# Kernel optimization log

Measured on AMD Instinct MI355X. Metric: run time of the kernel, lower is better.

The kernel has to match this reference:

```python
import jax, jax.numpy as jnp
import numpy as np

NUM_HEADS = 8
KERNEL = 7  # kernel_size (kh == kw == 7), dilation 1, non-causal


def _na_indices(L, k):
    # NATTEN neighborhood: window start clamped so the kxk window stays in-bounds
    starts = jnp.clip(jnp.arange(L) - k // 2, 0, L - k)  # [L]
    return starts[:, None] + jnp.arange(k)               # [L, k]


def setup_inputs() -> dict:
    key = jax.random.key(0)
    k1, k2, k3 = jax.random.split(key, 3)
    B, H, W, C = 1, 64, 128, 256
    x = jax.random.normal(k1, (B, H, W, C), dtype=jnp.float32)
    # weights stored as [in, out] so y = x @ w + b (equivalent to torch Linear math)
    w_qkv = jax.random.normal(k2, (C, 3 * C), dtype=jnp.float32) * 0.02
    b_qkv = jnp.zeros((3 * C,), dtype=jnp.float32)
    w_proj = jax.random.normal(k3, (C, C), dtype=jnp.float32) * 0.02
    b_proj = jnp.zeros((C,), dtype=jnp.float32)
    return {"x": x, "w_qkv": w_qkv, "b_qkv": b_qkv, "w_proj": w_proj, "b_proj": b_proj}


def reference(x, w_qkv, b_qkv, w_proj, b_proj):
    B, H, W, C = x.shape
    nh = NUM_HEADS
    hd = C // nh
    scale = hd ** -0.5
    kk = KERNEL

    qkv = (x @ w_qkv + b_qkv).reshape(B, H, W, 3, nh, hd)
    q = qkv[:, :, :, 0]  # [B,H,W,nh,hd]
    k = qkv[:, :, :, 1]
    v = qkv[:, :, :, 2]

    ih = _na_indices(H, kk)  # [H,kk]
    iw = _na_indices(W, kk)  # [W,kk]

    # gather K/V neighborhoods: [B,H,kh,W,kw,nh,hd]
    k_win = k[:, ih][:, :, :, iw]
    v_win = v[:, ih][:, :, :, iw]

    # scores: query vs its kh*kw neighbors
    attn = jnp.einsum('bhwnd,bhpwqnd->bhwnpq', q * scale, k_win)  # [B,H,W,nh,kh,kw]
    attn = jax.nn.softmax(attn.reshape(B, H, W, nh, kk * kk), axis=-1)
    attn = attn.reshape(B, H, W, nh, kk, kk)

    out = jnp.einsum('bhwnpq,bhpwqnd->bhwnd', attn, v_win)  # [B,H,W,nh,hd]
    out = out.reshape(B, H, W, C)
    return out @ w_proj + b_proj
```

## Files before the change

### kernel.cpp

```cpp
#include <hip/hip_runtime.h>
#include <cmath>

#define HH 64
#define WW 128
#define CC 256
#define NHEAD 8
#define HDIM 32
#define NPIX (HH*WW)
#define QKV_N (3*CC)

typedef __attribute__((ext_vector_type(8))) short short8v;
typedef __attribute__((ext_vector_type(4))) short short4v;
typedef __attribute__((ext_vector_type(4))) float f32x4;
typedef unsigned int u32;

__device__ __forceinline__ short f2bf(float f) {
    unsigned int u = __builtin_bit_cast(unsigned int, f);
    u += 0x7fffu + ((u >> 16) & 1u);
    return (short)(u >> 16);
}

__global__ __launch_bounds__(256)
void prep(const float* __restrict__ x, const float* __restrict__ w_qkv,
          const float* __restrict__ w_proj, short* __restrict__ x_bf,
          short* __restrict__ wqkv_t, short* __restrict__ wproj_t)
{
    __shared__ float tile[32][33];
    const int b = blockIdx.x;
    if (b < 1024) {
        const int i = b * 256 + threadIdx.x;
        float4 a = ((const float4*)x)[i * 2];
        float4 c = ((const float4*)x)[i * 2 + 1];
        short8v o;
        o[0] = f2bf(a.x); o[1] = f2bf(a.y); o[2] = f2bf(a.z); o[3] = f2bf(a.w);
        o[4] = f2bf(c.x); o[5] = f2bf(c.y); o[6] = f2bf(c.z); o[7] = f2bf(c.w);
        ((short8v*)x_bf)[i] = o;
        return;
    }
    const float* src; short* dst; int N, idx;
    if (b < 1216) { idx = b - 1024; src = w_qkv;  dst = wqkv_t;  N = QKV_N; }
    else          { idx = b - 1216; src = w_proj; dst = wproj_t; N = CC;    }
    const int nbx = N / 32;
    const int bn = (idx % nbx) * 32;
    const int bk = (idx / nbx) * 32;
    const int tx = threadIdx.x & 31, ty = threadIdx.x >> 5;
#pragma unroll
    for (int i = 0; i < 32; i += 8)
        tile[ty + i][tx] = src[(size_t)(bk + ty + i) * N + bn + tx];
    __syncthreads();
#pragma unroll
    for (int i = 0; i < 32; i += 8)
        dst[(size_t)(bn + ty + i) * CC + bk + tx] = f2bf(tile[tx][ty + i]);
}

template<int BM, int BN, bool OUT32>
__global__ __launch_bounds__(256)
void gemm_bf(const short* __restrict__ A, const short* __restrict__ Bt,
             const float* __restrict__ bias, void* __restrict__ Cv,
             int M, int N, int K)
{
    constexpr int BK  = 32;
    constexpr int NGA = BM * BK / 2048;
    constexpr int NGB = BN * BK / 2048;
    __shared__ short As[2][BM * BK];
    __shared__ short Bs[2][BN * BK];

    const int tid  = threadIdx.x;
    const int lane = tid & 63;
    const int wave = tid >> 6;
    constexpr int WM = BM / 2, WN = BN / 2;
    constexpr int FM = WM / 16, FN = WN / 16;
    const int wm0 = (wave >> 1) * WM;
    const int wn0 = (wave & 1) * WN;
    const int bm = blockIdx.x * BM, bn = blockIdx.y * BN;
    const int l15 = lane & 15, l4 = lane >> 4;

    f32x4 acc[FM][FN];
#pragma unroll
    for (int i = 0; i < FM; ++i)
#pragma unroll
        for (int j = 0; j < FN; ++j) acc[i][j] = (f32x4){0.f, 0.f, 0.f, 0.f};

    auto stage = [&](int buf, int t) {
#pragma unroll
        for (int i = 0; i < NGA; ++i) {
            const int g = tid + 256 * i;
            __builtin_amdgcn_global_load_lds(
                (const __attribute__((address_space(1))) u32*)
                    (A + (size_t)(bm + (g >> 2)) * K + t * BK + (g & 3) * 8),
                (__attribute__((address_space(3))) u32*)&As[buf][g * 8],
                16, 0, 0);
        }
#pragma unroll
        for (int i = 0; i < NGB; ++i) {
            const int g = tid + 256 * i;
            __builtin_amdgcn_global_load_lds(
                (const __attribute__((address_space(1))) u32*)
                    (Bt + (size_t)(bn + (g >> 2)) * K + t * BK + (g & 3) * 8),
                (__attribute__((address_space(3))) u32*)&Bs[buf][g * 8],
                16, 0, 0);
        }
    };

    stage(0, 0);
    const int NT = K / BK;

    for (int t = 0; t < NT; ++t) {
        const int cur = t & 1;
        __syncthreads();
        if (t + 1 < NT) stage(cur ^ 1, t + 1);

        short8v af[FM], bf[FN];
#pragma unroll
        for (int fm = 0; fm < FM; ++fm)
            af[fm] = *(const short8v*)&As[cur][(wm0 + fm * 16 + l15) * BK + l4 * 8];
#pragma unroll
        for (int fn = 0; fn < FN; ++fn)
            bf[fn] = *(const short8v*)&Bs[cur][(wn0 + fn * 16 + l15) * BK + l4 * 8];
#pragma unroll
        for (int fm = 0; fm < FM; ++fm)
#pragma unroll
            for (int fn = 0; fn < FN; ++fn)
                acc[fm][fn] = __builtin_amdgcn_mfma_f32_16x16x32_bf16(
                    af[fm], bf[fn], acc[fm][fn], 0, 0, 0);
    }

    const int col0 = bn + wn0 + l15;
    const int row0 = bm + wm0 + l4 * 4;
#pragma unroll
    for (int fn = 0; fn < FN; ++fn) {
        const float bv = bias[col0 + fn * 16];
#pragma unroll
        for (int fm = 0; fm < FM; ++fm)
#pragma unroll
            for (int r = 0; r < 4; ++r) {
                const size_t off = (size_t)(row0 + fm * 16 + r) * N + col0 + fn * 16;
                if (OUT32) ((float*)Cv)[off] = acc[fm][fn][r] + bv;
                else       ((short*)Cv)[off] = f2bf(acc[fm][fn][r] + bv);
            }
    }
}

#define KSLOT 248
#define LDK   40
#define VSLOT 264

__global__ __launch_bounds__(256)
void na_mfma(const short* __restrict__ qkv, short* __restrict__ attn)
{
    __shared__ short Ksh[KSLOT * LDK];
    __shared__ short Vsh[32 * VSLOT];

    const int x0 = blockIdx.x * 16;
    const int y0 = blockIdx.y * 4;
    const int head = blockIdx.z;
    const int tid = threadIdx.x, lane = tid & 63, w = tid >> 6;
    const int rs  = min(max(y0 - 3, 0), HH - 7);
    const int wsx = x0 - 3;

    for (int idx = tid; idx < 880; idx += 256) {
        int g = idx & 3, rc = idx >> 2;
        int i = rc / 22, c = rc - i * 22;
        int yy = rs + i, xx = wsx + c;
        if (yy < HH && (unsigned)xx < WW) {
            *(short8v*)&Ksh[(i * 24 + c) * LDK + g * 8] =
                *(const short8v*)(qkv + (size_t)(yy * WW + xx) * QKV_N
                                  + CC + head * HDIM + g * 8);
        }
    }
    for (int idx = tid; idx < 264; idx += 256) {
        int g = idx & 3, q2 = idx >> 2;
        int i = q2 / 6, cq = q2 - i * 6;
        int yy = rs + i;
        short8v vv[4];
#pragma unroll
        for (int j = 0; j < 4; ++j) {
            int c = cq * 4 + j, xx = wsx + c;
            if (yy < HH && c < 22 && (unsigned)xx < WW)
                vv[j] = *(const short8v*)(qkv + (size_t)(yy * WW + xx) * QKV_N
                                          + 2 * CC + head * HDIM + g * 8);
            else {
                short8v z = {0,0,0,0,0,0,0,0};
                vv[j] = z;
            }
        }
#pragma unroll
        for (int jd = 0; jd < 8; ++jd) {
            short4v s4 = {vv[0][jd], vv[1][jd], vv[2][jd], vv[3][jd]};
            *(short4v*)&Vsh[(g * 8 + jd) * VSLOT + i * 24 + cq * 4] = s4;
        }
    }

    const int l15 = lane & 15, l4 = lane >> 4;
    const int y = y0 + w;
    short8v qf = *(const short8v*)(qkv + (size_t)(y * WW + x0 + l15) * QKV_N
                                   + head * HDIM + l4 * 8);
    __syncthreads();

    const int wbase = (min(max(y - 3, 0), HH - 7) - rs) * 24;

    f32x4 sacc[11];
#pragma unroll
    for (int kc = 0; kc < 11; ++kc) {
        short8v kf = *(const short8v*)&Ksh[(wbase + kc * 16 + l15) * LDK + l4 * 8];
        f32x4 z = {0.f, 0.f, 0.f, 0.f};
        sacc[kc] = __builtin_amdgcn_mfma_f32_16x16x32_bf16(kf, qf, z, 0, 0, 0);
    }

    const int xq = x0 + l15;
    const int cw = min(max(xq - 3, 0), WW - 7) - wsx;
    const float scale = 0.17677669529663687f;
    float lsum = 0.f;
#pragma unroll
    for (int kc = 0; kc < 11; ++kc) {
#pragma unroll
        for (int r = 0; r < 4; ++r) {
            int kl = kc * 16 + l4 * 4 + r;
            int row = kl / 24;
            int c = kl - row * 24;
            bool valid = (row < 7) && (c >= cw) && (c <= cw + 6);
            float e = valid ? __expf(sacc[kc][r] * scale) : 0.f;
            sacc[kc][r] = e;
            lsum += e;
        }
    }
    lsum += __shfl_xor(lsum, 16);
    lsum += __shfl_xor(lsum, 32);
    const float inv = 1.0f / lsum;

    short4v pf[12];
#pragma unroll
    for (int kc = 0; kc < 11; ++kc) {
        short4v pk;
#pragma unroll
        for (int r = 0; r < 4; ++r) pk[r] = f2bf(sacc[kc][r] * inv);
        pf[kc] = pk;
    }
    pf[11] = (short4v){0, 0, 0, 0};

    const int src0 = ((l4 & 1) << 5) + l15;
    const int src1 = src0 + 16;
    const bool hi = (l4 & 2) != 0;
    f32x4 oacc[2];
    oacc[0] = (f32x4){0.f, 0.f, 0.f, 0.f};
    oacc[1] = (f32x4){0.f, 0.f, 0.f, 0.f};
#pragma unroll
    for (int kc2 = 0; kc2 < 6; ++kc2) {
        int lo0 = ((const int*)&pf[2 * kc2])[0];
        int lo1 = ((const int*)&pf[2 * kc2])[1];
        int hi0 = ((const int*)&pf[2 * kc2 + 1])[0];
        int hi1 = ((const int*)&pf[2 * kc2 + 1])[1];
        int a0 = __shfl(lo0, src0), a1 = __shfl(lo1, src0);
        int a2 = __shfl(lo0, src1), a3 = __shfl(lo1, src1);
        int b0 = __shfl(hi0, src0), b1 = __shfl(hi1, src0);
        int b2 = __shfl(hi0, src1), b3 = __shfl(hi1, src1);
        int w0 = hi ? b0 : a0, w1 = hi ? b1 : a1;
        int w2 = hi ? b2 : a2, w3 = hi ? b3 : a3;
        int wv[4] = {w0, w1, w2, w3};
        short8v bfrag = *(const short8v*)wv;
#pragma unroll
        for (int nc = 0; nc < 2; ++nc) {
            short8v vf = *(const short8v*)&Vsh[(nc * 16 + l15) * VSLOT
                                               + wbase + kc2 * 32 + l4 * 8];
            oacc[nc] = __builtin_amdgcn_mfma_f32_16x16x32_bf16(vf, bfrag, oacc[nc], 0, 0, 0);
        }
    }

    short* op = attn + (size_t)(y * WW + x0 + l15) * CC + head * HDIM;
#pragma unroll
    for (int nc = 0; nc < 2; ++nc) {
        short4v o;
#pragma unroll
        for (int r = 0; r < 4; ++r) o[r] = f2bf(oacc[nc][r]);
        *(short4v*)(op + nc * 16 + l4 * 4) = o;
    }
}

extern "C" void kernel_launch(void* const* d_in, const int* in_sizes, int n_in,
                              void* d_out, int out_size, void* d_ws, size_t ws_size,
                              hipStream_t stream)
{
    const float* x      = (const float*)d_in[0];
    const float* w_qkv  = (const float*)d_in[1];
    const float* b_qkv  = (const float*)d_in[2];
    const float* w_proj = (const float*)d_in[3];
    const float* b_proj = (const float*)d_in[4];
    float* out = (float*)d_out;

    char* ws = (char*)d_ws;
    short* qkv_bf  = (short*)ws;
    short* attn_bf = (short*)(ws + 12582912);
    short* x_bf    = (short*)(ws + 16777216);
    short* wqkv_t  = (short*)(ws + 20971520);
    short* wproj_t = (short*)(ws + 21364736);

    prep<<<dim3(1280), dim3(256), 0, stream>>>(x, w_qkv, w_proj,
                                               x_bf, wqkv_t, wproj_t);

    gemm_bf<128, 128, false><<<dim3(NPIX / 128, QKV_N / 128), dim3(256), 0, stream>>>(
        x_bf, wqkv_t, b_qkv, qkv_bf, NPIX, QKV_N, CC);

    na_mfma<<<dim3(WW / 16, HH / 4, NHEAD), dim3(256), 0, stream>>>(qkv_bf, attn_bf);

    gemm_bf<64, 128, true><<<dim3(NPIX / 64, CC / 128), dim3(256), 0, stream>>>(
        attn_bf, wproj_t, b_proj, out, NPIX, CC, CC);
}
```

Before: 41.62 us.

## Fuse x bf16 conversion into QKV GEMM, use head-major QKV layout, swizzle LDS

The fp32-to-bf16 conversion of x moves out of the prep kernel and into the QKV GEMM, which loads fp32 A tiles, converts them in registers and stores them to LDS. This removes a full write and reread of x in bf16. The QKV output is written head-major ([3*nh][NPIX][32]) so the neighborhood attention kernel reads contiguous 64-byte rows per pixel. Both GEMMs add an XOR swizzle on the LDS layout to cut bank conflicts. The QKV GEMM now uses 64x128 tiles with a single-buffered A tile and an extra barrier, and its scattered 2-byte stores into the head-major layout may hurt write efficiency.

```diff
diff --git a/kernel.cpp b/kernel.cpp
--- a/kernel.cpp
+++ b/kernel.cpp
@@ -9,6 +9,10 @@
 #define NPIX (HH*WW)
 #define QKV_N (3*CC)
 
+#define KSLOT 248
+#define LDK   40
+#define VSLOT 264
+
 typedef __attribute__((ext_vector_type(8))) short short8v;
 typedef __attribute__((ext_vector_type(4))) short short4v;
 typedef __attribute__((ext_vector_type(4))) float f32x4;
@@ -21,25 +25,14 @@
 }
 
 __global__ __launch_bounds__(256)
-void prep(const float* __restrict__ x, const float* __restrict__ w_qkv,
-          const float* __restrict__ w_proj, short* __restrict__ x_bf,
-          short* __restrict__ wqkv_t, short* __restrict__ wproj_t)
+void prep_w(const float* __restrict__ w_qkv, const float* __restrict__ w_proj,
+            short* __restrict__ wq_t, short* __restrict__ wp_t)
 {
     __shared__ float tile[32][33];
-    const int b = blockIdx.x;
-    if (b < 1024) {
-        const int i = b * 256 + threadIdx.x;
-        float4 a = ((const float4*)x)[i * 2];
-        float4 c = ((const float4*)x)[i * 2 + 1];
-        short8v o;
-        o[0] = f2bf(a.x); o[1] = f2bf(a.y); o[2] = f2bf(a.z); o[3] = f2bf(a.w);
-        o[4] = f2bf(c.x); o[5] = f2bf(c.y); o[6] = f2bf(c.z); o[7] = f2bf(c.w);
-        ((short8v*)x_bf)[i] = o;
-        return;
-    }
-    const float* src; short* dst; int N, idx;
-    if (b < 1216) { idx = b - 1024; src = w_qkv;  dst = wqkv_t;  N = QKV_N; }
-    else          { idx = b - 1216; src = w_proj; dst = wproj_t; N = CC;    }
+    int idx = blockIdx.x;
+    const float* src; short* dst; int N;
+    if (idx < 192) { src = w_qkv;  dst = wq_t; N = QKV_N; }
+    else { idx -= 192; src = w_proj; dst = wp_t; N = CC; }
     const int nbx = N / 32;
     const int bn = (idx % nbx) * 32;
     const int bk = (idx / nbx) * 32;
@@ -53,74 +46,153 @@
         dst[(size_t)(bn + ty + i) * CC + bk + tx] = f2bf(tile[tx][ty + i]);
 }
 
-template<int BM, int BN, bool OUT32>
 __global__ __launch_bounds__(256)
-void gemm_bf(const short* __restrict__ A, const short* __restrict__ Bt,
-             const float* __restrict__ bias, void* __restrict__ Cv,
-             int M, int N, int K)
-{
-    constexpr int BK  = 32;
-    constexpr int NGA = BM * BK / 2048;
-    constexpr int NGB = BN * BK / 2048;
-    __shared__ short As[2][BM * BK];
-    __shared__ short Bs[2][BN * BK];
-
-    const int tid  = threadIdx.x;
-    const int lane = tid & 63;
-    const int wave = tid >> 6;
-    constexpr int WM = BM / 2, WN = BN / 2;
-    constexpr int FM = WM / 16, FN = WN / 16;
-    const int wm0 = (wave >> 1) * WM;
-    const int wn0 = (wave & 1) * WN;
-    const int bm = blockIdx.x * BM, bn = blockIdx.y * BN;
+void gemm_qkv(const float* __restrict__ A, const short* __restrict__ Bt,
+              const float* __restrict__ bias, short* __restrict__ Cp)
+{
+    __shared__ short As[64 * 40];
+    __shared__ short Bs[2][128 * 32];
+
+    const int tid = threadIdx.x, lane = tid & 63, wave = tid >> 6;
+    const int wm0 = (wave >> 1) * 32, wn0 = (wave & 1) * 64;
+    const int bm = blockIdx.x * 64, bn = blockIdx.y * 128;
     const int l15 = lane & 15, l4 = lane >> 4;
-
-    f32x4 acc[FM][FN];
-#pragma unroll
-    for (int i = 0; i < FM; ++i)
-#pragma unroll
-        for (int j = 0; j < FN; ++j) acc[i][j] = (f32x4){0.f, 0.f, 0.f, 0.f};
-
-    auto stage = [&](int buf, int t) {
-#pragma unroll
-        for (int i = 0; i < NGA; ++i) {
+    const int arow = tid >> 2, akoff = (tid & 3) * 8;
+
+    f32x4 acc[2][4];
+#pragma unroll
+    for (int i = 0; i < 2; ++i)
+#pragma unroll
+        for (int j = 0; j < 4; ++j) acc[i][j] = (f32x4){0.f, 0.f, 0.f, 0.f};
+
+    auto stageB = [&](int buf, int t) {
+#pragma unroll
+        for (int i = 0; i < 2; ++i) {
             const int g = tid + 256 * i;
+            const int row = g >> 2, gr = g & 3;
             __builtin_amdgcn_global_load_lds(
                 (const __attribute__((address_space(1))) u32*)
-                    (A + (size_t)(bm + (g >> 2)) * K + t * BK + (g & 3) * 8),
-                (__attribute__((address_space(3))) u32*)&As[buf][g * 8],
-                16, 0, 0);
-        }
-#pragma unroll
-        for (int i = 0; i < NGB; ++i) {
-            const int g = tid + 256 * i;
+                    (Bt + (size_t)(bn + row) * CC + t * 32 + ((gr ^ (row & 3)) * 8)),
+                (__attribute__((address_space(3))) u32*)&Bs[buf][g * 8], 16, 0, 0);
+        }
+    };
+
+    float4 a0, a1;
+    {
+        const float* p = A + (size_t)(bm + arow) * CC + akoff;
+        a0 = *(const float4*)p; a1 = *(const float4*)(p + 4);
+    }
+    stageB(0, 0);
+
+    for (int t = 0; t < 8; ++t) {
+        const int cur = t & 1;
+        __syncthreads();
+        {
+            short8v w;
+            w[0] = f2bf(a0.x); w[1] = f2bf(a0.y); w[2] = f2bf(a0.z); w[3] = f2bf(a0.w);
+            w[4] = f2bf(a1.x); w[5] = f2bf(a1.y); w[6] = f2bf(a1.z); w[7] = f2bf(a1.w);
+            *(short8v*)&As[arow * 40 + akoff] = w;
+        }
+        __syncthreads();
+        if (t + 1 < 8) {
+            const float* p = A + (size_t)(bm + arow) * CC + (t + 1) * 32 + akoff;
+            a0 = *(const float4*)p; a1 = *(const float4*)(p + 4);
+            stageB(cur ^ 1, t + 1);
+        }
+
+        short8v af[2], bf[4];
+#pragma unroll
+        for (int fm = 0; fm < 2; ++fm)
+            af[fm] = *(const short8v*)&As[(wm0 + fm * 16 + l15) * 40 + l4 * 8];
+#pragma unroll
+        for (int fn = 0; fn < 4; ++fn) {
+            const int row = wn0 + fn * 16 + l15;
+            bf[fn] = *(const short8v*)&Bs[cur][row * 32 + ((l4 ^ (row & 3)) * 8)];
+        }
+#pragma unroll
+        for (int fm = 0; fm < 2; ++fm)
+#pragma unroll
+            for (int fn = 0; fn < 4; ++fn)
+                acc[fm][fn] = __builtin_amdgcn_mfma_f32_16x16x32_bf16(
+                    af[fm], bf[fn], acc[fm][fn], 0, 0, 0);
+    }
+
+    const int col0 = bn + wn0 + l15;
+    const int row0 = bm + wm0 + l4 * 4;
+#pragma unroll
+    for (int fn = 0; fn < 4; ++fn) {
+        const int cc = col0 + fn * 16;
+        const float bv = bias[cc];
+#pragma unroll
+        for (int fm = 0; fm < 2; ++fm)
+#pragma unroll
+            for (int r = 0; r < 4; ++r) {
+                const int rr = row0 + fm * 16 + r;
+                Cp[((size_t)(cc >> 5) * NPIX + rr) * HDIM + (cc & 31)] =
+                    f2bf(acc[fm][fn][r] + bv);
+            }
+    }
+}
+
+__global__ __launch_bounds__(256)
+void gemm_proj(const short* __restrict__ A, const short* __restrict__ Bt,
+               const float* __restrict__ bias, float* __restrict__ C)
+{
+    __shared__ short As[2][64 * 32];
+    __shared__ short Bs[2][128 * 32];
+
+    const int tid = threadIdx.x, lane = tid & 63, wave = tid >> 6;
+    const int wm0 = (wave >> 1) * 32, wn0 = (wave & 1) * 64;
+    const int bm = blockIdx.x * 64, bn = blockIdx.y * 128;
+    const int l15 = lane & 15, l4 = lane >> 4;
+
+    f32x4 acc[2][4];
+#pragma unroll
+    for (int i = 0; i < 2; ++i)
+#pragma unroll
+        for (int j = 0; j < 4; ++j) acc[i][j] = (f32x4){0.f, 0.f, 0.f, 0.f};
+
+    auto stage = [&](int buf, int t) {
+        {
+            const int row = tid >> 2, gr = tid & 3;
             __builtin_amdgcn_global_load_lds(
                 (const __attribute__((address_space(1))) u32*)
-                    (Bt + (size_t)(bn + (g >> 2)) * K + t * BK + (g & 3) * 8),
-                (__attribute__((address_space(3))) u32*)&Bs[buf][g * 8],
-                16, 0, 0);
+                    (A + (size_t)(bm + row) * CC + t * 32 + ((gr ^ (row & 3)) * 8)),
+                (__attribute__((address_space(3))) u32*)&As[buf][tid * 8], 16, 0, 0);
+        }
+#pragma unroll
+        for (int i = 0; i < 2; ++i) {
+            const int g = tid + 256 * i;
+            const int row = g >> 2, gr = g & 3;
+            __builtin_amdgcn_global_load_lds(
+                (const __attribute__((address_space(1))) u32*)
+                    (Bt + (size_t)(bn + row) * CC + t * 32 + ((gr ^ (row & 3)) * 8)),
+                (__attribute__((address_space(3))) u32*)&Bs[buf][g * 8], 16, 0, 0);
         }
     };
 
     stage(0, 0);
-    const int NT = K / BK;
-
-    for (int t = 0; t < NT; ++t) {
+
+    for (int t = 0; t < 8; ++t) {
         const int cur = t & 1;
         __syncthreads();
-        if (t + 1 < NT) stage(cur ^ 1, t + 1);
-
-        short8v af[FM], bf[FN];
-#pragma unroll
-        for (int fm = 0; fm < FM; ++fm)
-            af[fm] = *(const short8v*)&As[cur][(wm0 + fm * 16 + l15) * BK + l4 * 8];
-#pragma unroll
-        for (int fn = 0; fn < FN; ++fn)
-            bf[fn] = *(const short8v*)&Bs[cur][(wn0 + fn * 16 + l15) * BK + l4 * 8];
-#pragma unroll
-        for (int fm = 0; fm < FM; ++fm)
-#pragma unroll
-            for (int fn = 0; fn < FN; ++fn)
+        if (t + 1 < 8) stage(cur ^ 1, t + 1);
+
+        short8v af[2], bf[4];
+#pragma unroll
+        for (int fm = 0; fm < 2; ++fm) {
+            const int row = wm0 + fm * 16 + l15;
+            af[fm] = *(const short8v*)&As[cur][row * 32 + ((l4 ^ (row & 3)) * 8)];
+        }
+#pragma unroll
+        for (int fn = 0; fn < 4; ++fn) {
+            const int row = wn0 + fn * 16 + l15;
+            bf[fn] = *(const short8v*)&Bs[cur][row * 32 + ((l4 ^ (row & 3)) * 8)];
+        }
+#pragma unroll
+        for (int fm = 0; fm < 2; ++fm)
+#pragma unroll
+            for (int fn = 0; fn < 4; ++fn)
                 acc[fm][fn] = __builtin_amdgcn_mfma_f32_16x16x32_bf16(
                     af[fm], bf[fn], acc[fm][fn], 0, 0, 0);
     }
@@ -128,22 +200,16 @@
     const int col0 = bn + wn0 + l15;
     const int row0 = bm + wm0 + l4 * 4;
 #pragma unroll
-    for (int fn = 0; fn < FN; ++fn) {
+    for (int fn = 0; fn < 4; ++fn) {
         const float bv = bias[col0 + fn * 16];
 #pragma unroll
-        for (int fm = 0; fm < FM; ++fm)
-#pragma unroll
-            for (int r = 0; r < 4; ++r) {
-                const size_t off = (size_t)(row0 + fm * 16 + r) * N + col0 + fn * 16;
-                if (OUT32) ((float*)Cv)[off] = acc[fm][fn][r] + bv;
-                else       ((short*)Cv)[off] = f2bf(acc[fm][fn][r] + bv);
-            }
-    }
-}
-
-#define KSLOT 248
-#define LDK   40
-#define VSLOT 264
+        for (int fm = 0; fm < 2; ++fm)
+#pragma unroll
+            for (int r = 0; r < 4; ++r)
+                C[(size_t)(row0 + fm * 16 + r) * CC + col0 + fn * 16] =
+                    acc[fm][fn][r] + bv;
+    }
+}
 
 __global__ __launch_bounds__(256)
 void na_mfma(const short* __restrict__ qkv, short* __restrict__ attn)
@@ -157,16 +223,17 @@
     const int tid = threadIdx.x, lane = tid & 63, w = tid >> 6;
     const int rs  = min(max(y0 - 3, 0), HH - 7);
     const int wsx = x0 - 3;
+    const short* Qp = qkv + (size_t)head * NPIX * HDIM;
+    const short* Kp = qkv + (size_t)(NHEAD + head) * NPIX * HDIM;
+    const short* Vp = qkv + (size_t)(2 * NHEAD + head) * NPIX * HDIM;
 
     for (int idx = tid; idx < 880; idx += 256) {
         int g = idx & 3, rc = idx >> 2;
         int i = rc / 22, c = rc - i * 22;
         int yy = rs + i, xx = wsx + c;
-        if (yy < HH && (unsigned)xx < WW) {
+        if (yy < HH && (unsigned)xx < WW)
             *(short8v*)&Ksh[(i * 24 + c) * LDK + g * 8] =
-                *(const short8v*)(qkv + (size_t)(yy * WW + xx) * QKV_N
-                                  + CC + head * HDIM + g * 8);
-        }
+                *(const short8v*)(Kp + (size_t)(yy * WW + xx) * HDIM + g * 8);
     }
     for (int idx = tid; idx < 264; idx += 256) {
         int g = idx & 3, q2 = idx >> 2;
@@ -177,8 +244,7 @@
         for (int j = 0; j < 4; ++j) {
             int c = cq * 4 + j, xx = wsx + c;
             if (yy < HH && c < 22 && (unsigned)xx < WW)
-                vv[j] = *(const short8v*)(qkv + (size_t)(yy * WW + xx) * QKV_N
-                                          + 2 * CC + head * HDIM + g * 8);
+                vv[j] = *(const short8v*)(Vp + (size_t)(yy * WW + xx) * HDIM + g * 8);
             else {
                 short8v z = {0,0,0,0,0,0,0,0};
                 vv[j] = z;
@@ -193,8 +259,7 @@
 
     const int l15 = lane & 15, l4 = lane >> 4;
     const int y = y0 + w;
-    short8v qf = *(const short8v*)(qkv + (size_t)(y * WW + x0 + l15) * QKV_N
-                                   + head * HDIM + l4 * 8);
+    short8v qf = *(const short8v*)(Qp + (size_t)(y * WW + x0 + l15) * HDIM + l4 * 8);
     __syncthreads();
 
     const int wbase = (min(max(y - 3, 0), HH - 7) - rs) * 24;
@@ -288,20 +353,18 @@
     float* out = (float*)d_out;
 
     char* ws = (char*)d_ws;
-    short* qkv_bf  = (short*)ws;
+    short* qkv_r   = (short*)ws;
     short* attn_bf = (short*)(ws + 12582912);
-    short* x_bf    = (short*)(ws + 16777216);
-    short* wqkv_t  = (short*)(ws + 20971520);
-    short* wproj_t = (short*)(ws + 21364736);
-
-    prep<<<dim3(1280), dim3(256), 0, stream>>>(x, w_qkv, w_proj,
-                                               x_bf, wqkv_t, wproj_t);
-
-    gemm_bf<128, 128, false><<<dim3(NPIX / 128, QKV_N / 128), dim3(256), 0, stream>>>(
-        x_bf, wqkv_t, b_qkv, qkv_bf, NPIX, QKV_N, CC);
-
-    na_mfma<<<dim3(WW / 16, HH / 4, NHEAD), dim3(256), 0, stream>>>(qkv_bf, attn_bf);
-
-    gemm_bf<64, 128, true><<<dim3(NPIX / 64, CC / 128), dim3(256), 0, stream>>>(
-        attn_bf, wproj_t, b_proj, out, NPIX, CC, CC);
-}
+    short* wq_t    = (short*)(ws + 16777216);
+    short* wp_t    = (short*)(ws + 17170432);
+
+    prep_w<<<dim3(256), dim3(256), 0, stream>>>(w_qkv, w_proj, wq_t, wp_t);
+
+    gemm_qkv<<<dim3(NPIX / 64, QKV_N / 128), dim3(256), 0, stream>>>(
+        x, wq_t, b_qkv, qkv_r);
+
+    na_mfma<<<dim3(WW / 16, HH / 4, NHEAD), dim3(256), 0, stream>>>(qkv_r, attn_bf);
+
+    gemm_proj<<<dim3(NPIX / 64, CC / 128), dim3(256), 0, stream>>>(
+        attn_bf, wp_t, b_proj, out);
+}
```

Result: slower. 43.89 us (+5.5%).
